# Kernel optimization log

Hardware: AMD Instinct MI355X
Metric: run time of the kernel (lower is better)

The kernel has to match this reference:

```python
import jax, jax.numpy as jnp
import numpy as np
from jax import lax

C = 256      # in_c == out_c == dim
NH = 8       # num_heads
K = 7        # depthwise pos-enc kernel
H1 = 512     # int(mlp_ratio * in_c) = 2.0 * 256
B, Hs, Ws = 2, 48, 48


def setup_inputs() -> dict:
    key = jax.random.key(0)
    ks = jax.random.split(key, 8)
    w = lambda k, shape: jax.random.normal(k, shape, jnp.float32) * 0.02
    return {
        "x": jax.random.normal(ks[0], (B, C, Hs, Ws), jnp.float32),
        # 1x1 convs stored as [out, in] (BN folded into weight+bias)
        "qk_w": w(ks[1], (2 * C, C)), "qk_b": jnp.zeros((2 * C,), jnp.float32),
        "v_w": w(ks[2], (C, C)),       "v_b": jnp.zeros((C,), jnp.float32),
        # depthwise positional encoding conv [C,1,K,K]
        "pe_w": w(ks[3], (C, 1, K, K)), "pe_b": jnp.zeros((C,), jnp.float32),
        "proj_w": w(ks[4], (C, C)),    "proj_b": jnp.zeros((C,), jnp.float32),
        # conv FFN: 1x1 (SiLU) -> 1x1 (no act)
        "fc1_w": w(ks[5], (H1, C)),    "fc1_b": jnp.zeros((H1,), jnp.float32),
        "fc2_w": w(ks[6], (C, H1)),    "fc2_b": jnp.zeros((C,), jnp.float32),
    }


def _c1(x, w, b):
    # 1x1 conv == per-pixel matmul
    return jnp.einsum('bchw,oc->bohw', x, w) + b[None, :, None, None]


def reference(x, qk_w, qk_b, v_w, v_b, pe_w, pe_b, proj_w, proj_b,
              fc1_w, fc1_b, fc2_w, fc2_b):
    Bb, Cc, Hh, Ww = x.shape
    hd = Cc // NH                 # head_dim = 32
    N = Hh * Ww
    scale = hd ** -0.5

    # ---- AttentionV2 ----
    qk = _c1(x, qk_w, qk_b).reshape(Bb, NH, 2 * hd, N)
    q, k = qk[:, :, :hd], qk[:, :, hd:]
    v_full = _c1(x, v_w, v_b)                      # [B,C,H,W]
    pe = lax.conv_general_dilated(
        v_full, pe_w, (1, 1), 'SAME', feature_group_count=Cc,
        dimension_numbers=('NCHW', 'OIHW', 'NCHW')) + pe_b[None, :, None, None]
    v = v_full.reshape(Bb, NH, hd, N)

    # attn = q^T @ k * scale ; softmax over keys
    attn = jax.nn.softmax(jnp.einsum('bhdn,bhdm->bhnm', q, k) * scale, axis=-1)
    o = jnp.einsum('bhdm,bhnm->bhdn', v, attn).reshape(Bb, Cc, Hh, Ww)
    attn_out = _c1(o + pe, proj_w, proj_b)

    # ---- block residuals + conv FFN (add=True) ----
    x1 = x + attn_out
    h = jax.nn.silu(_c1(x1, fc1_w, fc1_b))         # Conv(in_c, hidden, 1, 1) with SiLU
    return x1 + _c1(h, fc2_w, fc2_b)               # Conv(hidden, out_c, 1, act=False)
```

## Files before the change

### kernel.cpp

```cpp
#include <hip/hip_runtime.h>
#include <hip/hip_bf16.h>

#define NCH 256
#define NHD 8
#define HD 32
#define NPIX 2304
#define H1DIM 512

typedef __attribute__((ext_vector_type(8))) __bf16 bf16x8;
typedef __attribute__((ext_vector_type(4))) float f32x4;

__global__ __launch_bounds__(256) void prep_k(
    const float* __restrict__ x,
    const float* __restrict__ w0, const float* __restrict__ w1,
    const float* __restrict__ w2, const float* __restrict__ w3,
    const float* __restrict__ w4,
    __bf16* __restrict__ Xb, __bf16* __restrict__ Wall) {
    const int tid = threadIdx.x;
    if (blockIdx.x < 288) {
        const int t = blockIdx.x;
        const int b = t / 144, r0 = t % 144;
        const int c0 = (r0 / 36) * 64, n0 = (r0 % 36) * 64;
        __shared__ float tile[64][65];
        const size_t sb = ((size_t)b * NCH + c0) * NPIX + n0;
#pragma unroll
        for (int i = 0; i < 16; ++i) {
            int idx = tid + i * 256;
            int rr = idx >> 6, cc = idx & 63;
            tile[rr][cc] = x[sb + (size_t)rr * NPIX + cc];
        }
        __syncthreads();
#pragma unroll
        for (int i = 0; i < 8; ++i) {
            int idx = tid + i * 256;
            int nn = idx >> 5, cp = (idx & 31) * 2;
            union { __bf16 h[2]; unsigned u; } pk;
            pk.h[0] = (__bf16)tile[cp][nn];
            pk.h[1] = (__bf16)tile[cp + 1][nn];
            *(unsigned*)&Xb[((size_t)b * NPIX + n0 + nn) * NCH + c0 + cp] = pk.u;
        }
    } else {
        int i = (blockIdx.x - 288) * 256 + tid;
        const float* src; int off;
        if (i < 32768)      { src = w0; off = i; }
        else if (i < 49152) { src = w1; off = i - 32768; }
        else if (i < 65536) { src = w2; off = i - 49152; }
        else if (i < 98304) { src = w3; off = i - 65536; }
        else                { src = w4; off = i - 98304; }
        float4 v = ((const float4*)src)[off];
        union { __bf16 h[4]; uint2 u; } pk;
        pk.h[0] = (__bf16)v.x; pk.h[1] = (__bf16)v.y;
        pk.h[2] = (__bf16)v.z; pk.h[3] = (__bf16)v.w;
        ((uint2*)Wall)[i] = pk.u;
    }
}

__global__ __launch_bounds__(256) void qkv_k(
    const __bf16* __restrict__ A, const __bf16* __restrict__ Wq,
    const __bf16* __restrict__ Wv, const float* __restrict__ qk_b,
    const float* __restrict__ v_b, __bf16* __restrict__ Qb,
    __bf16* __restrict__ Kf, float* __restrict__ v_bu,
    __bf16* __restrict__ Vf) {
    const int tid = threadIdx.x;
    const int wave = tid >> 6, lane = tid & 63;
    const int l16 = lane & 15, quad = lane >> 4;
    const int m0 = blockIdx.x * 64 + wave * 16;
    const int b = blockIdx.z;
    const bool isv = blockIdx.y >= 32;
    const int oc0 = (isv ? (blockIdx.y - 32) : blockIdx.y) * 16;
    const __bf16* W = isv ? Wv : Wq;

    const __bf16* aptr = A + ((size_t)b * NPIX + m0 + l16) * NCH + quad * 8;
    const __bf16* bptr = W + (size_t)(oc0 + l16) * NCH + quad * 8;

    f32x4 acc = {0.f, 0.f, 0.f, 0.f};
#pragma unroll 8
    for (int k = 0; k < NCH; k += 32) {
        bf16x8 af = *(const bf16x8*)(aptr + k);
        bf16x8 bf = *(const bf16x8*)(bptr + k);
        acc = __builtin_amdgcn_mfma_f32_16x16x32_bf16(af, bf, acc, 0, 0, 0);
    }

    const int oc = oc0 + l16;
    const int mb = m0 + quad * 4;

    if (!isv) {
        const float bb = qk_b[oc];
        const int h = oc0 >> 6;
        const int bh = b * NHD + h;
        const int dd = (oc0 & 16) + l16;
        if ((oc0 & 32) == 0) {
            const float qs = 0.17677669529663689f * 1.4426950408889634f;
#pragma unroll
            for (int r = 0; r < 4; ++r)
                Qb[((size_t)bh * NPIX + mb + r) * 32 + dd] = (__bf16)((acc[r] + bb) * qs);
        } else {
            __bf16* kp = Kf + ((size_t)(bh * 144 + (m0 >> 4)) * 64 + (dd >> 3) * 16 + quad * 4) * 8 + (dd & 7);
#pragma unroll
            for (int r = 0; r < 4; ++r) kp[r * 8] = (__bf16)(acc[r] + bb);
        }
    } else {
        const float bb = v_b[oc];
        const int h = oc0 >> 5;
        const int bh = b * NHD + h;
        const int half = (oc0 >> 4) & 1;
        const size_t fb = ((size_t)b * NCH + oc) * NPIX + mb;
        float4 vf_; float* vp = &vf_.x;
        union { __bf16 hh[4]; uint2 u; } pk;
#pragma unroll
        for (int r = 0; r < 4; ++r) {
            float v = acc[r] + bb;
            vp[r] = v; pk.hh[r] = (__bf16)v;
        }
        *(float4*)&v_bu[fb] = vf_;
        *(uint2*)&Vf[((size_t)(bh * 144 + (m0 >> 4)) * 64 + lane) * 8 + half * 4] = pk.u;
    }
}

template <int IC, int OC, int MODE>
__global__ __launch_bounds__(256) void convmm_k(
    const __bf16* __restrict__ A, const __bf16* __restrict__ W,
    const float* __restrict__ bias, const float* __restrict__ resid,
    float* __restrict__ out_f, __bf16* __restrict__ out_b) {
    const int tid = threadIdx.x;
    const int wave = tid >> 6, lane = tid & 63;
    const int l16 = lane & 15, quad = lane >> 4;
    const int m0 = blockIdx.x * 64 + wave * 16;
    const int oc0 = blockIdx.y * 16;
    const int b = blockIdx.z;

    const __bf16* aptr = A + ((size_t)b * NPIX + m0 + l16) * IC + quad * 8;
    const __bf16* bptr = W + (size_t)(oc0 + l16) * IC + quad * 8;

    f32x4 acc = {0.f, 0.f, 0.f, 0.f};
#pragma unroll 8
    for (int k = 0; k < IC; k += 32) {
        bf16x8 af = *(const bf16x8*)(aptr + k);
        bf16x8 bf = *(const bf16x8*)(bptr + k);
        acc = __builtin_amdgcn_mfma_f32_16x16x32_bf16(af, bf, acc, 0, 0, 0);
    }

    const int oc = oc0 + l16;
    const int mb = m0 + quad * 4;
    const float bb = bias[oc];

    if constexpr (MODE == 2) {
        const size_t fb = ((size_t)b * OC + oc) * NPIX + mb;
        float4 xr = *(const float4*)&resid[fb];
        const float* xp = &xr.x;
        float4 vf_; float* vp = &vf_.x;
#pragma unroll
        for (int r = 0; r < 4; ++r) {
            float v = acc[r] + bb + xp[r];
            vp[r] = v;
            out_b[((size_t)b * NPIX + mb + r) * OC + oc] = (__bf16)v;
        }
        *(float4*)&out_f[fb] = vf_;
    } else if constexpr (MODE == 3) {
#pragma unroll
        for (int r = 0; r < 4; ++r) {
            float v = acc[r] + bb;
            v = v / (1.f + __expf(-v));
            out_b[((size_t)b * NPIX + mb + r) * OC + oc] = (__bf16)v;
        }
    } else {
        const size_t fb = ((size_t)b * OC + oc) * NPIX + mb;
        float4 xr = *(const float4*)&resid[fb];
        const float* xp = &xr.x;
        float4 vf_; float* vp = &vf_.x;
#pragma unroll
        for (int r = 0; r < 4; ++r) vp[r] = acc[r] + bb + xp[r];
        *(float4*)&out_f[fb] = vf_;
    }
}

__global__ __launch_bounds__(256) void dwconv_k(const float* __restrict__ vb,
                                                const float* __restrict__ pw,
                                                const float* __restrict__ pb,
                                                float* __restrict__ pe) {
    const int c = blockIdx.x, b = blockIdx.y, tid = threadIdx.x;
    __shared__ float plane[NPIX];
    __shared__ float wk[49];
    const size_t base = ((size_t)b * NCH + c) * NPIX;
    for (int i = tid; i < NPIX; i += 256) plane[i] = vb[base + i];
    if (tid < 49) wk[tid] = pw[c * 49 + tid];
    float bb = pb[c];
    __syncthreads();
    for (int p = tid; p < NPIX; p += 256) {
        int y = p / 48, x = p - y * 48;
        float s = bb;
#pragma unroll
        for (int ky = 0; ky < 7; ++ky) {
            int yy = y + ky - 3;
            if ((unsigned)yy < 48u) {
#pragma unroll
                for (int kx = 0; kx < 7; ++kx) {
                    int xx = x + kx - 3;
                    if ((unsigned)xx < 48u) s += wk[ky * 7 + kx] * plane[yy * 48 + xx];
                }
            }
        }
        pe[base + p] = s;
    }
}

__global__ __launch_bounds__(512) void attn6_k(const __bf16* __restrict__ Qb,
                                               const __bf16* __restrict__ Kf,
                                               const __bf16* __restrict__ Vf,
                                               const float* __restrict__ pe,
                                               __bf16* __restrict__ opb) {
    const int tid = threadIdx.x;
    const int wave = tid >> 6, lane = tid & 63;
    const int l16 = lane & 15, quad = lane >> 4;
    const int qb = blockIdx.x * 32;
    const int h = blockIdx.y, b = blockIdx.z;
    const int bh = b * NHD + h;

    __shared__ float o_s[8][32][33];
    __shared__ float l_s[8][32];

    bf16x8 b_q0 = *(const bf16x8*)(Qb + ((size_t)bh * NPIX + qb + l16) * 32 + quad * 8);
    bf16x8 b_q1 = *(const bf16x8*)(Qb + ((size_t)bh * NPIX + qb + 16 + l16) * 32 + quad * 8);

    const __bf16* kf = Kf + ((size_t)(bh * 144 + wave * 18) * 64 + lane) * 8;
    const __bf16* vf = Vf + ((size_t)(bh * 144 + wave * 18) * 64 + lane) * 8;

    f32x4 o00 = {0.f,0.f,0.f,0.f}, o01 = {0.f,0.f,0.f,0.f};
    f32x4 o10 = {0.f,0.f,0.f,0.f}, o11 = {0.f,0.f,0.f,0.f};
    f32x4 l0 = {0.f,0.f,0.f,0.f}, l1 = {0.f,0.f,0.f,0.f};

#pragma unroll 3
    for (int t = 0; t < 18; ++t) {
        bf16x8 a_k = *(const bf16x8*)(kf + (size_t)t * 512);
        bf16x8 va  = *(const bf16x8*)(vf + (size_t)t * 512);
        f32x4 z = {0.f, 0.f, 0.f, 0.f};
        f32x4 s0 = __builtin_amdgcn_mfma_f32_16x16x32_bf16(a_k, b_q0, z, 0, 0, 0);
        f32x4 s1 = __builtin_amdgcn_mfma_f32_16x16x32_bf16(a_k, b_q1, z, 0, 0, 0);
        f32x4 p0, p1;
#pragma unroll
        for (int r = 0; r < 4; ++r) {
            p0[r] = __builtin_amdgcn_exp2f(s0[r]);
            p1[r] = __builtin_amdgcn_exp2f(s1[r]);
        }
        l0 += p0; l1 += p1;
        bf16x8 b0lo = {}, b0hi = {}, b1lo = {}, b1hi = {};
#pragma unroll
        for (int r = 0; r < 4; ++r) {
            __bf16 c0 = (__bf16)p0[r], c1 = (__bf16)p1[r];
            b0lo[r] = c0; b0hi[4 + r] = c0;
            b1lo[r] = c1; b1hi[4 + r] = c1;
        }
        o00 = __builtin_amdgcn_mfma_f32_16x16x32_bf16(va, b0lo, o00, 0, 0, 0);
        o01 = __builtin_amdgcn_mfma_f32_16x16x32_bf16(va, b0hi, o01, 0, 0, 0);
        o10 = __builtin_amdgcn_mfma_f32_16x16x32_bf16(va, b1lo, o10, 0, 0, 0);
        o11 = __builtin_amdgcn_mfma_f32_16x16x32_bf16(va, b1hi, o11, 0, 0, 0);
    }

    float ls0 = l0[0] + l0[1] + l0[2] + l0[3];
    ls0 += __shfl_xor(ls0, 16); ls0 += __shfl_xor(ls0, 32);
    float ls1 = l1[0] + l1[1] + l1[2] + l1[3];
    ls1 += __shfl_xor(ls1, 16); ls1 += __shfl_xor(ls1, 32);

#pragma unroll
    for (int r = 0; r < 4; ++r) {
        o_s[wave][quad * 4 + r][l16]           = o00[r];
        o_s[wave][16 + quad * 4 + r][l16]      = o01[r];
        o_s[wave][quad * 4 + r][16 + l16]      = o10[r];
        o_s[wave][16 + quad * 4 + r][16 + l16] = o11[r];
    }
    if (quad == 0) { l_s[wave][l16] = ls0; l_s[wave][16 + l16] = ls1; }
    __syncthreads();

    const int q = tid & 31;
    const int d0 = (tid >> 5) * 2;
    float l = 0.f;
#pragma unroll
    for (int w = 0; w < 8; ++w) l += l_s[w][q];
    const float inv = 1.f / l;
    float v0 = 0.f, v1 = 0.f;
#pragma unroll
    for (int w = 0; w < 8; ++w) {
        v0 += o_s[w][d0][q];
        v1 += o_s[w][d0 + 1][q];
    }
    const int n = qb + q;
    const int ch = h * HD + d0;
    v0 = v0 * inv + pe[((size_t)b * NCH + ch) * NPIX + n];
    v1 = v1 * inv + pe[((size_t)b * NCH + ch + 1) * NPIX + n];
    union { __bf16 hh[2]; unsigned u; } pk;
    pk.hh[0] = (__bf16)v0; pk.hh[1] = (__bf16)v1;
    *(unsigned*)&opb[((size_t)b * NPIX + n) * NCH + ch] = pk.u;
}

extern "C" void kernel_launch(void* const* d_in, const int* in_sizes, int n_in,
                              void* d_out, int out_size, void* d_ws, size_t ws_size,
                              hipStream_t stream) {
    const float* x    = (const float*)d_in[0];
    const float* qk_w = (const float*)d_in[1];
    const float* qk_b = (const float*)d_in[2];
    const float* v_w  = (const float*)d_in[3];
    const float* v_b  = (const float*)d_in[4];
    const float* pe_w = (const float*)d_in[5];
    const float* pe_b = (const float*)d_in[6];
    const float* pj_w = (const float*)d_in[7];
    const float* pj_b = (const float*)d_in[8];
    const float* f1_w = (const float*)d_in[9];
    const float* f1_b = (const float*)d_in[10];
    const float* f2_w = (const float*)d_in[11];
    const float* f2_b = (const float*)d_in[12];
    float* out = (float*)d_out;

    const int B = 2;
    const size_t plane = (size_t)NCH * NPIX;
    const size_t bp = (size_t)B * plane;

    float* v_bu  = (float*)d_ws;
    float* pe_bu = v_bu + bp;
    float* x1_f  = pe_bu + bp;
    __bf16* Xb   = (__bf16*)(x1_f + bp);
    __bf16* opb  = Xb + bp;
    __bf16* x1b  = opb + bp;
    __bf16* hb   = x1b + bp;
    __bf16* Qb   = hb + 2 * bp;
    __bf16* Kf   = Qb + bp;
    __bf16* Vf   = Kf + bp;
    __bf16* Wall = Vf + bp;
    __bf16* Wq = Wall;
    __bf16* Wv = Wall + 131072;
    __bf16* Wp = Wall + 196608;
    __bf16* W1 = Wall + 262144;
    __bf16* W2 = Wall + 393216;

    prep_k<<<800, 256, 0, stream>>>(x, qk_w, v_w, pj_w, f1_w, f2_w, Xb, Wall);
    qkv_k<<<dim3(36, 48, B), 256, 0, stream>>>(Xb, Wq, Wv, qk_b, v_b, Qb, Kf, v_bu, Vf);
    dwconv_k<<<dim3(NCH, B), 256, 0, stream>>>(v_bu, pe_w, pe_b, pe_bu);
    attn6_k<<<dim3(NPIX / 32, NHD, B), 512, 0, stream>>>(Qb, Kf, Vf, pe_bu, opb);
    convmm_k<256, 256, 2><<<dim3(36, 16, B), 256, 0, stream>>>(
        opb, Wp, pj_b, x, x1_f, x1b);
    convmm_k<256, 512, 3><<<dim3(36, 32, B), 256, 0, stream>>>(
        x1b, W1, f1_b, nullptr, nullptr, hb);
    convmm_k<512, 256, 4><<<dim3(36, 16, B), 256, 0, stream>>>(
        hb, W2, f2_b, x1_f, out, nullptr);
}
```

Measured before the change: 210.7 us.

## Remap grid indices so blocks sharing a head or pixel tile land on one XCD

Launches every kernel on a flattened 1D grid and decodes the block index so that blockIdx.x & 7 (the XCD round-robin slot) selects the head, channel group or pixel tile. Blocks on the same XCD then touch the same head's Q/K/V or the same activation rows, which is meant to raise per-XCD L2 hit rates on MI355X. In the conv GEMMs each wave now owns a different 16-channel slice of a shared pixel tile rather than a different pixel tile of a shared channel slice. The main risk is that the new index arithmetic, and any gain from the new access pattern, depends on the hardware really dispatching blocks round-robin across XCDs.

New measurement: 209.3 us. About the same (-0.6%).

```diff
diff --git a/kernel.cpp b/kernel.cpp
--- a/kernel.cpp
+++ b/kernel.cpp
@@ -64,10 +64,16 @@
     const int tid = threadIdx.x;
     const int wave = tid >> 6, lane = tid & 63;
     const int l16 = lane & 15, quad = lane >> 4;
-    const int m0 = blockIdx.x * 64 + wave * 16;
-    const int b = blockIdx.z;
-    const bool isv = blockIdx.y >= 32;
-    const int oc0 = (isv ? (blockIdx.y - 32) : blockIdx.y) * 16;
+    const int h = blockIdx.x & 7;
+    const int u = blockIdx.x >> 3;
+    const int tau = u * 4 + wave;
+    const int px = tau % 144;
+    const int rest = tau / 144;
+    const int b = rest & 1;
+    const int sub = rest >> 1;
+    const int m0 = px * 16;
+    const bool isv = sub >= 4;
+    const int oc0 = isv ? (32 * h + 16 * (sub - 4)) : (64 * h + 16 * sub);
     const __bf16* W = isv ? Wv : Wq;
 
     const __bf16* aptr = A + ((size_t)b * NPIX + m0 + l16) * NCH + quad * 8;
@@ -86,7 +92,6 @@
 
     if (!isv) {
         const float bb = qk_b[oc];
-        const int h = oc0 >> 6;
         const int bh = b * NHD + h;
         const int dd = (oc0 & 16) + l16;
         if ((oc0 & 32) == 0) {
@@ -95,13 +100,12 @@
             for (int r = 0; r < 4; ++r)
                 Qb[((size_t)bh * NPIX + mb + r) * 32 + dd] = (__bf16)((acc[r] + bb) * qs);
         } else {
-            __bf16* kp = Kf + ((size_t)(bh * 144 + (m0 >> 4)) * 64 + (dd >> 3) * 16 + quad * 4) * 8 + (dd & 7);
+            __bf16* kp = Kf + ((size_t)(bh * 144 + px) * 64 + (dd >> 3) * 16 + quad * 4) * 8 + (dd & 7);
 #pragma unroll
             for (int r = 0; r < 4; ++r) kp[r * 8] = (__bf16)(acc[r] + bb);
         }
     } else {
         const float bb = v_b[oc];
-        const int h = oc0 >> 5;
         const int bh = b * NHD + h;
         const int half = (oc0 >> 4) & 1;
         const size_t fb = ((size_t)b * NCH + oc) * NPIX + mb;
@@ -113,11 +117,11 @@
             vp[r] = v; pk.hh[r] = (__bf16)v;
         }
         *(float4*)&v_bu[fb] = vf_;
-        *(uint2*)&Vf[((size_t)(bh * 144 + (m0 >> 4)) * 64 + lane) * 8 + half * 4] = pk.u;
-    }
-}
-
-template <int IC, int OC, int MODE>
+        *(uint2*)&Vf[((size_t)(bh * 144 + px) * 64 + lane) * 8 + half * 4] = pk.u;
+    }
+}
+
+template <int IC, int OC, int OCQ, int MODE>
 __global__ __launch_bounds__(256) void convmm_k(
     const __bf16* __restrict__ A, const __bf16* __restrict__ W,
     const float* __restrict__ bias, const float* __restrict__ resid,
@@ -125,9 +129,14 @@
     const int tid = threadIdx.x;
     const int wave = tid >> 6, lane = tid & 63;
     const int l16 = lane & 15, quad = lane >> 4;
-    const int m0 = blockIdx.x * 64 + wave * 16;
-    const int oc0 = blockIdx.y * 16;
-    const int b = blockIdx.z;
+    const int xcd = blockIdx.x & 7;
+    const int u = blockIdx.x >> 3;
+    const int ocq = u % OCQ;
+    const int rest = u / OCQ;
+    const int m8 = rest % 18;
+    const int b = rest / 18;
+    const int m0 = (m8 * 8 + xcd) * 16;
+    const int oc0 = (ocq * 4 + wave) * 16;
 
     const __bf16* aptr = A + ((size_t)b * NPIX + m0 + l16) * IC + quad * 8;
     const __bf16* bptr = W + (size_t)(oc0 + l16) * IC + quad * 8;
@@ -178,7 +187,10 @@
                                                 const float* __restrict__ pw,
                                                 const float* __restrict__ pb,
                                                 float* __restrict__ pe) {
-    const int c = blockIdx.x, b = blockIdx.y, tid = threadIdx.x;
+    const int tid = threadIdx.x;
+    const int r = (int)blockIdx.x >> 3;
+    const int c = (blockIdx.x & 7) * 32 + (r & 31);
+    const int b = r >> 5;
     __shared__ float plane[NPIX];
     __shared__ float wk[49];
     const size_t base = ((size_t)b * NCH + c) * NPIX;
@@ -212,8 +224,11 @@
     const int tid = threadIdx.x;
     const int wave = tid >> 6, lane = tid & 63;
     const int l16 = lane & 15, quad = lane >> 4;
-    const int qb = blockIdx.x * 32;
-    const int h = blockIdx.y, b = blockIdx.z;
+    const int h = blockIdx.x & 7;
+    const int r0 = (int)blockIdx.x >> 3;
+    const int qt = r0 % 72;
+    const int b = r0 / 72;
+    const int qb = qt * 32;
     const int bh = b * NHD + h;
 
     __shared__ float o_s[8][32][33];
@@ -332,13 +347,10 @@
     __bf16* W2 = Wall + 393216;
 
     prep_k<<<800, 256, 0, stream>>>(x, qk_w, v_w, pj_w, f1_w, f2_w, Xb, Wall);
-    qkv_k<<<dim3(36, 48, B), 256, 0, stream>>>(Xb, Wq, Wv, qk_b, v_b, Qb, Kf, v_bu, Vf);
-    dwconv_k<<<dim3(NCH, B), 256, 0, stream>>>(v_bu, pe_w, pe_b, pe_bu);
-    attn6_k<<<dim3(NPIX / 32, NHD, B), 512, 0, stream>>>(Qb, Kf, Vf, pe_bu, opb);
-    convmm_k<256, 256, 2><<<dim3(36, 16, B), 256, 0, stream>>>(
-        opb, Wp, pj_b, x, x1_f, x1b);
-    convmm_k<256, 512, 3><<<dim3(36, 32, B), 256, 0, stream>>>(
-        x1b, W1, f1_b, nullptr, nullptr, hb);
-    convmm_k<512, 256, 4><<<dim3(36, 16, B), 256, 0, stream>>>(
-        hb, W2, f2_b, x1_f, out, nullptr);
-}
+    qkv_k<<<3456, 256, 0, stream>>>(Xb, Wq, Wv, qk_b, v_b, Qb, Kf, v_bu, Vf);
+    dwconv_k<<<512, 256, 0, stream>>>(v_bu, pe_w, pe_b, pe_bu);
+    attn6_k<<<1152, 512, 0, stream>>>(Qb, Kf, Vf, pe_bu, opb);
+    convmm_k<256, 256, 4, 2><<<1152, 256, 0, stream>>>(opb, Wp, pj_b, x, x1_f, x1b);
+    convmm_k<256, 512, 8, 3><<<2304, 256, 0, stream>>>(x1b, W1, f1_b, nullptr, nullptr, hb);
+    convmm_k<512, 256, 4, 4><<<1152, 256, 0, stream>>>(hb, W2, f2_b, x1_f, out, nullptr);
+}
```

## Register-block GEMM and attention kernels to reuse weight and K/V fragments

Applied to the files above, without the earlier changes.

The 1x1-conv GEMM kernels now give each wave two 16-pixel row tiles that share one weight fragment, and the waves in a block split output channels instead of pixels. The attention kernel processes 64 queries per block instead of 32, so each loaded K/V fragment feeds four query groups, which halves K/V traffic and the number of blocks. The aim is less redundant global loading per MFMA, at the cost of more accumulator registers and a larger shared-memory reduction buffer, which may lower occupancy.

Measured after the change: 210.0 us. No clear change (-0.3%).

```diff
diff --git a/kernel.cpp b/kernel.cpp
--- a/kernel.cpp
+++ b/kernel.cpp
@@ -64,56 +64,62 @@
     const int tid = threadIdx.x;
     const int wave = tid >> 6, lane = tid & 63;
     const int l16 = lane & 15, quad = lane >> 4;
-    const int m0 = blockIdx.x * 64 + wave * 16;
+    const int m0 = blockIdx.x * 32;
+    const int idx = blockIdx.y * 4 + wave;
     const int b = blockIdx.z;
-    const bool isv = blockIdx.y >= 32;
-    const int oc0 = (isv ? (blockIdx.y - 32) : blockIdx.y) * 16;
+    const bool isv = idx >= 32;
+    const int oc0 = (isv ? idx - 32 : idx) * 16;
     const __bf16* W = isv ? Wv : Wq;
 
     const __bf16* aptr = A + ((size_t)b * NPIX + m0 + l16) * NCH + quad * 8;
     const __bf16* bptr = W + (size_t)(oc0 + l16) * NCH + quad * 8;
 
-    f32x4 acc = {0.f, 0.f, 0.f, 0.f};
+    f32x4 acc0 = {0.f,0.f,0.f,0.f}, acc1 = {0.f,0.f,0.f,0.f};
 #pragma unroll 8
     for (int k = 0; k < NCH; k += 32) {
-        bf16x8 af = *(const bf16x8*)(aptr + k);
         bf16x8 bf = *(const bf16x8*)(bptr + k);
-        acc = __builtin_amdgcn_mfma_f32_16x16x32_bf16(af, bf, acc, 0, 0, 0);
+        bf16x8 a0 = *(const bf16x8*)(aptr + k);
+        bf16x8 a1 = *(const bf16x8*)(aptr + (size_t)16 * NCH + k);
+        acc0 = __builtin_amdgcn_mfma_f32_16x16x32_bf16(a0, bf, acc0, 0, 0, 0);
+        acc1 = __builtin_amdgcn_mfma_f32_16x16x32_bf16(a1, bf, acc1, 0, 0, 0);
     }
 
     const int oc = oc0 + l16;
-    const int mb = m0 + quad * 4;
-
-    if (!isv) {
-        const float bb = qk_b[oc];
-        const int h = oc0 >> 6;
-        const int bh = b * NHD + h;
-        const int dd = (oc0 & 16) + l16;
-        if ((oc0 & 32) == 0) {
-            const float qs = 0.17677669529663689f * 1.4426950408889634f;
-#pragma unroll
-            for (int r = 0; r < 4; ++r)
-                Qb[((size_t)bh * NPIX + mb + r) * 32 + dd] = (__bf16)((acc[r] + bb) * qs);
+#pragma unroll
+    for (int mh = 0; mh < 2; ++mh) {
+        const f32x4 acc = mh ? acc1 : acc0;
+        const int m0h = m0 + mh * 16;
+        const int mb = m0h + quad * 4;
+        const int px16 = m0h >> 4;
+        if (!isv) {
+            const float bb = qk_b[oc];
+            const int bh = b * NHD + (oc0 >> 6);
+            const int dd = (oc0 & 16) + l16;
+            if ((oc0 & 32) == 0) {
+                const float qs = 0.17677669529663689f * 1.4426950408889634f;
+#pragma unroll
+                for (int r = 0; r < 4; ++r)
+                    Qb[((size_t)bh * NPIX + mb + r) * 32 + dd] = (__bf16)((acc[r] + bb) * qs);
+            } else {
+                __bf16* kp = Kf + ((size_t)(bh * 144 + px16) * 64 + (dd >> 3) * 16 + quad * 4) * 8 + (dd & 7);
+#pragma unroll
+                for (int r = 0; r < 4; ++r) kp[r * 8] = (__bf16)(acc[r] + bb);
+            }
         } else {
-            __bf16* kp = Kf + ((size_t)(bh * 144 + (m0 >> 4)) * 64 + (dd >> 3) * 16 + quad * 4) * 8 + (dd & 7);
-#pragma unroll
-            for (int r = 0; r < 4; ++r) kp[r * 8] = (__bf16)(acc[r] + bb);
-        }
-    } else {
-        const float bb = v_b[oc];
-        const int h = oc0 >> 5;
-        const int bh = b * NHD + h;
-        const int half = (oc0 >> 4) & 1;
-        const size_t fb = ((size_t)b * NCH + oc) * NPIX + mb;
-        float4 vf_; float* vp = &vf_.x;
-        union { __bf16 hh[4]; uint2 u; } pk;
-#pragma unroll
-        for (int r = 0; r < 4; ++r) {
-            float v = acc[r] + bb;
-            vp[r] = v; pk.hh[r] = (__bf16)v;
-        }
-        *(float4*)&v_bu[fb] = vf_;
-        *(uint2*)&Vf[((size_t)(bh * 144 + (m0 >> 4)) * 64 + lane) * 8 + half * 4] = pk.u;
+            const float bb = v_b[oc];
+            const int bh = b * NHD + (oc0 >> 5);
+            const int half = (oc0 >> 4) & 1;
+            const size_t fb = ((size_t)b * NCH + oc) * NPIX + mb;
+            float4 vf_; float* vp = &vf_.x;
+            union { __bf16 hh[4]; uint2 u; } pk;
+#pragma unroll
+            for (int r = 0; r < 4; ++r) {
+                float v = acc[r] + bb;
+                vp[r] = v; pk.hh[r] = (__bf16)v;
+            }
+            *(float4*)&v_bu[fb] = vf_;
+            *(uint2*)&Vf[((size_t)(bh * 144 + px16) * 64 + lane) * 8 + half * 4] = pk.u;
+        }
     }
 }
 
@@ -125,52 +131,57 @@
     const int tid = threadIdx.x;
     const int wave = tid >> 6, lane = tid & 63;
     const int l16 = lane & 15, quad = lane >> 4;
-    const int m0 = blockIdx.x * 64 + wave * 16;
-    const int oc0 = blockIdx.y * 16;
+    const int m0 = blockIdx.x * 32;
+    const int oc0 = (blockIdx.y * 4 + wave) * 16;
     const int b = blockIdx.z;
 
     const __bf16* aptr = A + ((size_t)b * NPIX + m0 + l16) * IC + quad * 8;
     const __bf16* bptr = W + (size_t)(oc0 + l16) * IC + quad * 8;
 
-    f32x4 acc = {0.f, 0.f, 0.f, 0.f};
+    f32x4 acc0 = {0.f,0.f,0.f,0.f}, acc1 = {0.f,0.f,0.f,0.f};
 #pragma unroll 8
     for (int k = 0; k < IC; k += 32) {
-        bf16x8 af = *(const bf16x8*)(aptr + k);
         bf16x8 bf = *(const bf16x8*)(bptr + k);
-        acc = __builtin_amdgcn_mfma_f32_16x16x32_bf16(af, bf, acc, 0, 0, 0);
+        bf16x8 a0 = *(const bf16x8*)(aptr + k);
+        bf16x8 a1 = *(const bf16x8*)(aptr + (size_t)16 * IC + k);
+        acc0 = __builtin_amdgcn_mfma_f32_16x16x32_bf16(a0, bf, acc0, 0, 0, 0);
+        acc1 = __builtin_amdgcn_mfma_f32_16x16x32_bf16(a1, bf, acc1, 0, 0, 0);
     }
 
     const int oc = oc0 + l16;
-    const int mb = m0 + quad * 4;
     const float bb = bias[oc];
-
-    if constexpr (MODE == 2) {
-        const size_t fb = ((size_t)b * OC + oc) * NPIX + mb;
-        float4 xr = *(const float4*)&resid[fb];
-        const float* xp = &xr.x;
-        float4 vf_; float* vp = &vf_.x;
-#pragma unroll
-        for (int r = 0; r < 4; ++r) {
-            float v = acc[r] + bb + xp[r];
-            vp[r] = v;
-            out_b[((size_t)b * NPIX + mb + r) * OC + oc] = (__bf16)v;
-        }
-        *(float4*)&out_f[fb] = vf_;
-    } else if constexpr (MODE == 3) {
-#pragma unroll
-        for (int r = 0; r < 4; ++r) {
-            float v = acc[r] + bb;
-            v = v / (1.f + __expf(-v));
-            out_b[((size_t)b * NPIX + mb + r) * OC + oc] = (__bf16)v;
-        }
-    } else {
-        const size_t fb = ((size_t)b * OC + oc) * NPIX + mb;
-        float4 xr = *(const float4*)&resid[fb];
-        const float* xp = &xr.x;
-        float4 vf_; float* vp = &vf_.x;
-#pragma unroll
-        for (int r = 0; r < 4; ++r) vp[r] = acc[r] + bb + xp[r];
-        *(float4*)&out_f[fb] = vf_;
+#pragma unroll
+    for (int mh = 0; mh < 2; ++mh) {
+        const f32x4 acc = mh ? acc1 : acc0;
+        const int mb = m0 + mh * 16 + quad * 4;
+        if constexpr (MODE == 2) {
+            const size_t fb = ((size_t)b * OC + oc) * NPIX + mb;
+            float4 xr = *(const float4*)&resid[fb];
+            const float* xp = &xr.x;
+            float4 vf_; float* vp = &vf_.x;
+#pragma unroll
+            for (int r = 0; r < 4; ++r) {
+                float v = acc[r] + bb + xp[r];
+                vp[r] = v;
+                out_b[((size_t)b * NPIX + mb + r) * OC + oc] = (__bf16)v;
+            }
+            *(float4*)&out_f[fb] = vf_;
+        } else if constexpr (MODE == 3) {
+#pragma unroll
+            for (int r = 0; r < 4; ++r) {
+                float v = acc[r] + bb;
+                v = v / (1.f + __expf(-v));
+                out_b[((size_t)b * NPIX + mb + r) * OC + oc] = (__bf16)v;
+            }
+        } else {
+            const size_t fb = ((size_t)b * OC + oc) * NPIX + mb;
+            float4 xr = *(const float4*)&resid[fb];
+            const float* xp = &xr.x;
+            float4 vf_; float* vp = &vf_.x;
+#pragma unroll
+            for (int r = 0; r < 4; ++r) vp[r] = acc[r] + bb + xp[r];
+            *(float4*)&out_f[fb] = vf_;
+        }
     }
 }
 
@@ -204,92 +215,91 @@
     }
 }
 
-__global__ __launch_bounds__(512) void attn6_k(const __bf16* __restrict__ Qb,
-                                               const __bf16* __restrict__ Kf,
-                                               const __bf16* __restrict__ Vf,
-                                               const float* __restrict__ pe,
-                                               __bf16* __restrict__ opb) {
+__global__ __launch_bounds__(512, 4) void attn7_k(const __bf16* __restrict__ Qb,
+                                                  const __bf16* __restrict__ Kf,
+                                                  const __bf16* __restrict__ Vf,
+                                                  const float* __restrict__ pe,
+                                                  __bf16* __restrict__ opb) {
     const int tid = threadIdx.x;
     const int wave = tid >> 6, lane = tid & 63;
     const int l16 = lane & 15, quad = lane >> 4;
-    const int qb = blockIdx.x * 32;
+    const int qb = blockIdx.x * 64;
     const int h = blockIdx.y, b = blockIdx.z;
     const int bh = b * NHD + h;
 
-    __shared__ float o_s[8][32][33];
-    __shared__ float l_s[8][32];
-
-    bf16x8 b_q0 = *(const bf16x8*)(Qb + ((size_t)bh * NPIX + qb + l16) * 32 + quad * 8);
-    bf16x8 b_q1 = *(const bf16x8*)(Qb + ((size_t)bh * NPIX + qb + 16 + l16) * 32 + quad * 8);
+    __shared__ float o_s[8][32][65];
+    __shared__ float l_s[8][64];
+
+    bf16x8 b_q[4];
+#pragma unroll
+    for (int g = 0; g < 4; ++g)
+        b_q[g] = *(const bf16x8*)(Qb + ((size_t)bh * NPIX + qb + g * 16 + l16) * 32 + quad * 8);
 
     const __bf16* kf = Kf + ((size_t)(bh * 144 + wave * 18) * 64 + lane) * 8;
     const __bf16* vf = Vf + ((size_t)(bh * 144 + wave * 18) * 64 + lane) * 8;
 
-    f32x4 o00 = {0.f,0.f,0.f,0.f}, o01 = {0.f,0.f,0.f,0.f};
-    f32x4 o10 = {0.f,0.f,0.f,0.f}, o11 = {0.f,0.f,0.f,0.f};
-    f32x4 l0 = {0.f,0.f,0.f,0.f}, l1 = {0.f,0.f,0.f,0.f};
-
-#pragma unroll 3
+    f32x4 oacc[4][2];
+    f32x4 lacc[4];
+#pragma unroll
+    for (int g = 0; g < 4; ++g) {
+        oacc[g][0] = {0.f,0.f,0.f,0.f};
+        oacc[g][1] = {0.f,0.f,0.f,0.f};
+        lacc[g] = {0.f,0.f,0.f,0.f};
+    }
+
+#pragma unroll 2
     for (int t = 0; t < 18; ++t) {
         bf16x8 a_k = *(const bf16x8*)(kf + (size_t)t * 512);
         bf16x8 va  = *(const bf16x8*)(vf + (size_t)t * 512);
-        f32x4 z = {0.f, 0.f, 0.f, 0.f};
-        f32x4 s0 = __builtin_amdgcn_mfma_f32_16x16x32_bf16(a_k, b_q0, z, 0, 0, 0);
-        f32x4 s1 = __builtin_amdgcn_mfma_f32_16x16x32_bf16(a_k, b_q1, z, 0, 0, 0);
-        f32x4 p0, p1;
-#pragma unroll
-        for (int r = 0; r < 4; ++r) {
-            p0[r] = __builtin_amdgcn_exp2f(s0[r]);
-            p1[r] = __builtin_amdgcn_exp2f(s1[r]);
-        }
-        l0 += p0; l1 += p1;
-        bf16x8 b0lo = {}, b0hi = {}, b1lo = {}, b1hi = {};
-#pragma unroll
-        for (int r = 0; r < 4; ++r) {
-            __bf16 c0 = (__bf16)p0[r], c1 = (__bf16)p1[r];
-            b0lo[r] = c0; b0hi[4 + r] = c0;
-            b1lo[r] = c1; b1hi[4 + r] = c1;
-        }
-        o00 = __builtin_amdgcn_mfma_f32_16x16x32_bf16(va, b0lo, o00, 0, 0, 0);
-        o01 = __builtin_amdgcn_mfma_f32_16x16x32_bf16(va, b0hi, o01, 0, 0, 0);
-        o10 = __builtin_amdgcn_mfma_f32_16x16x32_bf16(va, b1lo, o10, 0, 0, 0);
-        o11 = __builtin_amdgcn_mfma_f32_16x16x32_bf16(va, b1hi, o11, 0, 0, 0);
-    }
-
-    float ls0 = l0[0] + l0[1] + l0[2] + l0[3];
-    ls0 += __shfl_xor(ls0, 16); ls0 += __shfl_xor(ls0, 32);
-    float ls1 = l1[0] + l1[1] + l1[2] + l1[3];
-    ls1 += __shfl_xor(ls1, 16); ls1 += __shfl_xor(ls1, 32);
-
-#pragma unroll
-    for (int r = 0; r < 4; ++r) {
-        o_s[wave][quad * 4 + r][l16]           = o00[r];
-        o_s[wave][16 + quad * 4 + r][l16]      = o01[r];
-        o_s[wave][quad * 4 + r][16 + l16]      = o10[r];
-        o_s[wave][16 + quad * 4 + r][16 + l16] = o11[r];
-    }
-    if (quad == 0) { l_s[wave][l16] = ls0; l_s[wave][16 + l16] = ls1; }
+#pragma unroll
+        for (int g = 0; g < 4; ++g) {
+            f32x4 z = {0.f, 0.f, 0.f, 0.f};
+            f32x4 s = __builtin_amdgcn_mfma_f32_16x16x32_bf16(a_k, b_q[g], z, 0, 0, 0);
+            f32x4 p;
+#pragma unroll
+            for (int r = 0; r < 4; ++r) p[r] = __builtin_amdgcn_exp2f(s[r]);
+            lacc[g] += p;
+            bf16x8 blo = {}, bhi = {};
+#pragma unroll
+            for (int r = 0; r < 4; ++r) {
+                __bf16 c = (__bf16)p[r];
+                blo[r] = c; bhi[4 + r] = c;
+            }
+            oacc[g][0] = __builtin_amdgcn_mfma_f32_16x16x32_bf16(va, blo, oacc[g][0], 0, 0, 0);
+            oacc[g][1] = __builtin_amdgcn_mfma_f32_16x16x32_bf16(va, bhi, oacc[g][1], 0, 0, 0);
+        }
+    }
+
+#pragma unroll
+    for (int g = 0; g < 4; ++g) {
+        float ls = lacc[g][0] + lacc[g][1] + lacc[g][2] + lacc[g][3];
+        ls += __shfl_xor(ls, 16); ls += __shfl_xor(ls, 32);
+        if (quad == 0) l_s[wave][g * 16 + l16] = ls;
+#pragma unroll
+        for (int half = 0; half < 2; ++half)
+#pragma unroll
+            for (int r = 0; r < 4; ++r)
+                o_s[wave][half * 16 + quad * 4 + r][g * 16 + l16] = oacc[g][half][r];
+    }
     __syncthreads();
 
-    const int q = tid & 31;
-    const int d0 = (tid >> 5) * 2;
+    const int q = lane;
+    const int d0 = wave * 4;
     float l = 0.f;
 #pragma unroll
     for (int w = 0; w < 8; ++w) l += l_s[w][q];
     const float inv = 1.f / l;
-    float v0 = 0.f, v1 = 0.f;
-#pragma unroll
-    for (int w = 0; w < 8; ++w) {
-        v0 += o_s[w][d0][q];
-        v1 += o_s[w][d0 + 1][q];
-    }
     const int n = qb + q;
-    const int ch = h * HD + d0;
-    v0 = v0 * inv + pe[((size_t)b * NCH + ch) * NPIX + n];
-    v1 = v1 * inv + pe[((size_t)b * NCH + ch + 1) * NPIX + n];
-    union { __bf16 hh[2]; unsigned u; } pk;
-    pk.hh[0] = (__bf16)v0; pk.hh[1] = (__bf16)v1;
-    *(unsigned*)&opb[((size_t)b * NPIX + n) * NCH + ch] = pk.u;
+    union { __bf16 hh[4]; uint2 u; } pk;
+#pragma unroll
+    for (int j = 0; j < 4; ++j) {
+        float v = 0.f;
+#pragma unroll
+        for (int w = 0; w < 8; ++w) v += o_s[w][d0 + j][q];
+        v = v * inv + pe[((size_t)b * NCH + h * HD + d0 + j) * NPIX + n];
+        pk.hh[j] = (__bf16)v;
+    }
+    *(uint2*)&opb[((size_t)b * NPIX + n) * NCH + h * HD + d0] = pk.u;
 }
 
 extern "C" void kernel_launch(void* const* d_in, const int* in_sizes, int n_in,
@@ -332,13 +342,10 @@
     __bf16* W2 = Wall + 393216;
 
     prep_k<<<800, 256, 0, stream>>>(x, qk_w, v_w, pj_w, f1_w, f2_w, Xb, Wall);
-    qkv_k<<<dim3(36, 48, B), 256, 0, stream>>>(Xb, Wq, Wv, qk_b, v_b, Qb, Kf, v_bu, Vf);
+    qkv_k<<<dim3(72, 12, B), 256, 0, stream>>>(Xb, Wq, Wv, qk_b, v_b, Qb, Kf, v_bu, Vf);
     dwconv_k<<<dim3(NCH, B), 256, 0, stream>>>(v_bu, pe_w, pe_b, pe_bu);
-    attn6_k<<<dim3(NPIX / 32, NHD, B), 512, 0, stream>>>(Qb, Kf, Vf, pe_bu, opb);
-    convmm_k<256, 256, 2><<<dim3(36, 16, B), 256, 0, stream>>>(
-        opb, Wp, pj_b, x, x1_f, x1b);
-    convmm_k<256, 512, 3><<<dim3(36, 32, B), 256, 0, stream>>>(
-        x1b, W1, f1_b, nullptr, nullptr, hb);
-    convmm_k<512, 256, 4><<<dim3(36, 16, B), 256, 0, stream>>>(
-        hb, W2, f2_b, x1_f, out, nullptr);
-}
+    attn7_k<<<dim3(36, NHD, B), 512, 0, stream>>>(Qb, Kf, Vf, pe_bu, opb);
+    convmm_k<256, 256, 2><<<dim3(72, 4, B), 256, 0, stream>>>(opb, Wp, pj_b, x, x1_f, x1b);
+    convmm_k<256, 512, 3><<<dim3(72, 8, B), 256, 0, stream>>>(x1b, W1, f1_b, nullptr, nullptr, hb);
+    convmm_k<512, 256, 4><<<dim3(72, 4, B), 256, 0, stream>>>(hb, W2, f2_b, x1_f, out, nullptr);
+}
```
